# Kernel tuning notes

Measured on AMD Instinct MI355X. Metric: run time of the kernel, lower is better.

## Reference

```python
import jax, jax.numpy as jnp
import numpy as np

N = 1024
EMB = 128
FC = 512


def setup_inputs() -> dict:
    key = jax.random.key(0)
    ks = jax.random.split(key, 13)
    s = 0.05
    return {
        "x": jax.random.normal(ks[0], (N, 2), jnp.float32),
        "w_rel0": jax.random.normal(ks[1], (EMB, 2), jnp.float32) * s,
        "b_rel0": jax.random.normal(ks[2], (EMB,), jnp.float32) * s,
        "w_root0": jax.random.normal(ks[3], (EMB, 2), jnp.float32) * s,
        "w_rel1": jax.random.normal(ks[4], (EMB, EMB), jnp.float32) * s,
        "b_rel1": jax.random.normal(ks[5], (EMB,), jnp.float32) * s,
        "w_root1": jax.random.normal(ks[6], (EMB, EMB), jnp.float32) * s,
        "lw0": jax.random.normal(ks[7], (FC, EMB), jnp.float32) * s,
        "lb0": jax.random.normal(ks[8], (FC,), jnp.float32) * s,
        "lw1": jax.random.normal(ks[9], (FC, FC), jnp.float32) * s,
        "lb1": jax.random.normal(ks[10], (FC,), jnp.float32) * s,
        "lw2": jax.random.normal(ks[11], (1, FC), jnp.float32) * s,
        "lb2": jax.random.normal(ks[12], (1,), jnp.float32) * s,
    }


def _sage(x, w_rel, b_rel, w_root):
    # DenseSAGEConv with adj = all-ones NxN: neighbor mean == global mean.
    # out = lin_rel(adj@x / deg) + lin_root(x); lin_root has no bias.
    agg = jnp.mean(x, axis=0, keepdims=True)            # (1, d_in)
    return agg @ w_rel.T + b_rel + x @ w_root.T          # (N, d_out)


def reference(x, w_rel0, b_rel0, w_root0, w_rel1, b_rel1, w_root1,
              lw0, lb0, lw1, lb1, lw2, lb2):
    h = jax.nn.relu(_sage(x, w_rel0, b_rel0, w_root0))    # (N, EMB)
    h = jax.nn.relu(_sage(h, w_rel1, b_rel1, w_root1))    # (N, EMB)
    # triu(ones, 1).nonzero() -> all pairs i < j (static, N known at trace time)
    ei, ej = np.triu_indices(h.shape[0], 1)
    e = h[ei] * h[ej]                                     # (E, EMB)
    o = jax.nn.relu(e @ lw0.T + lb0)                      # (E, FC)
    o = jax.nn.relu(o @ lw1.T + lb1)                      # (E, FC)
    o = o @ lw2.T + lb2                                   # (E, 1)
    return jax.nn.sigmoid(o)[:, 0]                        # (E,)
```

## Files before the change

### kernel.cpp

```cpp
#include <hip/hip_runtime.h>
#include <hip/hip_bf16.h>
#include <math.h>

#define NN 1024
#define EMB 128
#define FC 512
#define NEDGE 523776
#define BM 64

typedef __attribute__((ext_vector_type(16))) float f32x16;
typedef __attribute__((ext_vector_type(8))) short bf16x8;
typedef __attribute__((ext_vector_type(4))) unsigned int u32x4;
typedef __attribute__((ext_vector_type(8))) int i32x8;

__device__ __forceinline__ float bf2f(unsigned short u) {
  union { unsigned int i; float f; } v; v.i = ((unsigned int)u) << 16; return v.f;
}
__device__ __forceinline__ unsigned short f2bf(float f) {
  return __builtin_bit_cast(unsigned short, __float2bfloat16(f));
}
__device__ __forceinline__ int cum_edges(int i) { return i * NN - ((i * (i + 1)) >> 1); }

__device__ __forceinline__ unsigned int pk4_fp8(float a, float b, float c, float d) {
  int v = __builtin_amdgcn_cvt_pk_fp8_f32(a, b, 0, false);
  v = __builtin_amdgcn_cvt_pk_fp8_f32(c, d, v, true);
  return (unsigned int)v;
}
#define MFMA32_L0(A,B,C) __builtin_amdgcn_mfma_scale_f32_32x32x64_f8f6f4((A),(B),(C),0,0,0,0x76767676,0,0x7f7f7f7f)
#define MFMA32_L1(A,B,C) __builtin_amdgcn_mfma_scale_f32_32x32x64_f8f6f4((A),(B),(C),0,0,0,0x72727272,0,0x7f7f7f7f)

__global__ void k_cvt_weights(const float* __restrict__ lw0, const float* __restrict__ lw1,
                              unsigned int* __restrict__ w0q, unsigned int* __restrict__ w1q) {
  int d = blockIdx.x * 256 + threadIdx.x;
  if (d < 16384) {
    int dw = d & 7, lane = (d >> 3) & 63, f = (d >> 9) & 1, kb = (d >> 10) & 1, wv = (d >> 11) & 7;
    int fc = wv*64 + f*32 + (lane & 31);
    int k  = kb*64 + (lane >> 5)*32 + dw*4;
    float4 s = *(const float4*)(lw0 + fc*EMB + k);
    w0q[d] = pk4_fp8(s.x*64.f, s.y*64.f, s.z*64.f, s.w*64.f);
  } else {
    int u = d - 16384;
    int dw = u & 7, lane = (u >> 3) & 63, f = (u >> 9) & 1, kb = (u >> 10) & 7, wv = (u >> 13) & 7;
    int fc = wv*64 + f*32 + (lane & 31);
    int k  = kb*64 + (lane >> 5)*32 + dw*4;
    float4 s = *(const float4*)(lw1 + fc*FC + k);
    w1q[u] = pk4_fp8(s.x*64.f, s.y*64.f, s.z*64.f, s.w*64.f);
  }
}

__global__ void k_mean_x(const float* __restrict__ x, float* __restrict__ mean0) {
  __shared__ float sx[256], sy[256];
  float ax = 0.f, ay = 0.f;
  for (int i = threadIdx.x; i < NN; i += 256) { ax += x[2*i]; ay += x[2*i+1]; }
  sx[threadIdx.x] = ax; sy[threadIdx.x] = ay;
  __syncthreads();
  for (int st = 128; st > 0; st >>= 1) {
    if (threadIdx.x < st) { sx[threadIdx.x] += sx[threadIdx.x+st]; sy[threadIdx.x] += sy[threadIdx.x+st]; }
    __syncthreads();
  }
  if (threadIdx.x == 0) { mean0[0] = sx[0] * (1.f/NN); mean0[1] = sy[0] * (1.f/NN); }
}

__global__ void k_sage0(const float* __restrict__ x, const float* __restrict__ wrel,
                        const float* __restrict__ brel, const float* __restrict__ wroot,
                        const float* __restrict__ mean0, float* __restrict__ h0) {
  int idx = blockIdx.x * 256 + threadIdx.x;
  int i = idx >> 7, c = idx & 127;
  float v = mean0[0]*wrel[2*c] + mean0[1]*wrel[2*c+1] + brel[c]
          + x[2*i]*wroot[2*c] + x[2*i+1]*wroot[2*c+1];
  h0[idx] = fmaxf(v, 0.f);
}

__global__ void k_mean_h0(const float* __restrict__ h0, float* __restrict__ mean1) {
  __shared__ float s[256];
  int c = blockIdx.x;
  float a = 0.f;
  for (int i = threadIdx.x; i < NN; i += 256) a += h0[i*EMB + c];
  s[threadIdx.x] = a;
  __syncthreads();
  for (int st = 128; st > 0; st >>= 1) {
    if (threadIdx.x < st) s[threadIdx.x] += s[threadIdx.x+st];
    __syncthreads();
  }
  if (threadIdx.x == 0) mean1[c] = s[0] * (1.f/NN);
}

__global__ void k_relc(const float* __restrict__ mean1, const float* __restrict__ wrel1,
                       const float* __restrict__ brel1, float* __restrict__ relc) {
  int c = threadIdx.x;
  float a = brel1[c];
  #pragma unroll 8
  for (int k = 0; k < EMB; ++k) a += mean1[k] * wrel1[c*EMB + k];
  relc[c] = a;
}

__global__ void k_sage1(const float* __restrict__ h0, const float* __restrict__ wroot1,
                        const float* __restrict__ relc, unsigned short* __restrict__ hb) {
  int idx = blockIdx.x * 256 + threadIdx.x;
  int i = idx >> 7, c = idx & 127;
  const float4* hr = (const float4*)(h0 + i*EMB);
  const float4* wr = (const float4*)(wroot1 + c*EMB);
  float a = relc[c];
  #pragma unroll 8
  for (int k = 0; k < EMB/4; ++k) {
    float4 h = hr[k], w = wr[k];
    a += h.x*w.x + h.y*w.y + h.z*w.z + h.w*w.w;
  }
  hb[idx] = f2bf(fmaxf(a, 0.f) * 32.0f);
}

__global__ __launch_bounds__(512, 4)
void k_edge_mlp(const unsigned short* __restrict__ hb,
                const unsigned int* __restrict__ w0q,
                const float* __restrict__ lb0,
                const unsigned int* __restrict__ w1q,
                const float* __restrict__ lb1,
                const float* __restrict__ lw2,
                const float* __restrict__ lb2,
                float* __restrict__ out) {
  __shared__ __align__(32) unsigned int e_lds[2048];
  __shared__ __align__(32) unsigned int o0_lds[8192];

  const int tid  = threadIdx.x;
  const int lane = tid & 63;
  const int wv   = tid >> 6;
  const int l31  = lane & 31;
  const int hi   = lane >> 5;
  const int blk  = blockIdx.x;
  const int fcb  = wv * 64;

  const char* w0w = (const char*)w0q + wv * 8192;
  const char* w1w = (const char*)w1q + wv * 32768;

  {
    int r = tid >> 3, q = tid & 7;
    int k = blk * BM + r;
    float s = sqrtf((float)(4190209 - 8*k));
    int i = (int)((2047.0f - s) * 0.5f);
    if (i < 0) i = 0;
    if (i > NN-2) i = NN-2;
    if (cum_edges(i+1) <= k) ++i;
    if (cum_edges(i+1) <= k) ++i;
    if (cum_edges(i) > k) --i;
    if (cum_edges(i) > k) --i;
    int j = k - cum_edges(i) + i + 1;
    const bf16x8* hi8 = (const bf16x8*)(hb + i*EMB + q*16);
    const bf16x8* hj8 = (const bf16x8*)(hb + j*EMB + q*16);
    float p[16];
    #pragma unroll
    for (int g = 0; g < 2; ++g) {
      bf16x8 a = hi8[g], b = hj8[g];
      #pragma unroll
      for (int u = 0; u < 8; ++u)
        p[g*8+u] = bf2f((unsigned short)a[u]) * bf2f((unsigned short)b[u]);
    }
    u32x4 d;
    #pragma unroll
    for (int u = 0; u < 4; ++u)
      d[u] = pk4_fp8(p[4*u], p[4*u+1], p[4*u+2], p[4*u+3]);
    int byt = (r>>5)*4096 + (q>>2)*2048 + ((q>>1)&1)*1024 + (r&31)*32 + (q&1)*16;
    *(u32x4*)((char*)e_lds + byt) = d;
  }
  __syncthreads();

  f32x16 acc[2][2];

  #pragma unroll
  for (int f = 0; f < 2; ++f)
    #pragma unroll
    for (int t = 0; t < 4; ++t) {
      float4 bv = *(const float4*)(lb0 + fcb + f*32 + t*8 + hi*4);
      #pragma unroll
      for (int e = 0; e < 2; ++e) {
        acc[e][f][4*t+0] = bv.x*128.f; acc[e][f][4*t+1] = bv.y*128.f;
        acc[e][f][4*t+2] = bv.z*128.f; acc[e][f][4*t+3] = bv.w*128.f;
      }
    }
  {
    const char* rbe = (const char*)e_lds + lane*32;
    #pragma unroll
    for (int kb = 0; kb < 2; ++kb) {
      i32x8 a0 = *(const i32x8*)(w0w + (kb*2+0)*2048 + lane*32);
      i32x8 a1 = *(const i32x8*)(w0w + (kb*2+1)*2048 + lane*32);
      i32x8 b0 = *(const i32x8*)(rbe + kb*2048);
      i32x8 b1 = *(const i32x8*)(rbe + 4096 + kb*2048);
      __builtin_amdgcn_s_setprio(1);
      acc[0][0] = MFMA32_L0(a0, b0, acc[0][0]);
      acc[0][1] = MFMA32_L0(a1, b0, acc[0][1]);
      acc[1][0] = MFMA32_L0(a0, b1, acc[1][0]);
      acc[1][1] = MFMA32_L0(a1, b1, acc[1][1]);
      __builtin_amdgcn_s_setprio(0);
    }
  }

  {
    char* ob = (char*)o0_lds + wv*2048 + l31*32 + hi*4;
    #pragma unroll
    for (int f = 0; f < 2; ++f)
      #pragma unroll
      for (int e = 0; e < 2; ++e)
        #pragma unroll
        for (int t = 0; t < 4; ++t) {
          unsigned int d = pk4_fp8(fmaxf(acc[e][f][4*t+0], 0.f),
                                   fmaxf(acc[e][f][4*t+1], 0.f),
                                   fmaxf(acc[e][f][4*t+2], 0.f),
                                   fmaxf(acc[e][f][4*t+3], 0.f));
          *(unsigned int*)(ob + e*16384 + f*1024 + t*8) = d;
        }
  }
  __syncthreads();

  #pragma unroll
  for (int f = 0; f < 2; ++f)
    #pragma unroll
    for (int t = 0; t < 4; ++t) {
      float4 bv = *(const float4*)(lb1 + fcb + f*32 + t*8 + hi*4);
      #pragma unroll
      for (int e = 0; e < 2; ++e) {
        acc[e][f][4*t+0] = bv.x; acc[e][f][4*t+1] = bv.y;
        acc[e][f][4*t+2] = bv.z; acc[e][f][4*t+3] = bv.w;
      }
    }
  {
    const char* rbo = (const char*)o0_lds + lane*32;
    #pragma unroll
    for (int kb = 0; kb < 8; ++kb) {
      i32x8 a0 = *(const i32x8*)(w1w + (kb*2+0)*2048 + lane*32);
      i32x8 a1 = *(const i32x8*)(w1w + (kb*2+1)*2048 + lane*32);
      i32x8 b0 = *(const i32x8*)(rbo + kb*2048);
      i32x8 b1 = *(const i32x8*)(rbo + 16384 + kb*2048);
      __builtin_amdgcn_s_setprio(1);
      acc[0][0] = MFMA32_L1(a0, b0, acc[0][0]);
      acc[0][1] = MFMA32_L1(a1, b0, acc[0][1]);
      acc[1][0] = MFMA32_L1(a0, b1, acc[1][0]);
      acc[1][1] = MFMA32_L1(a1, b1, acc[1][1]);
      __builtin_amdgcn_s_setprio(0);
    }
  }

  {
    float rs0 = 0.f, rs1 = 0.f;
    #pragma unroll
    for (int f = 0; f < 2; ++f)
      #pragma unroll
      for (int t = 0; t < 4; ++t) {
        float4 l2v = *(const float4*)(lw2 + fcb + f*32 + t*8 + hi*4);
        rs0 += fmaxf(acc[0][f][4*t+0], 0.f) * l2v.x;
        rs0 += fmaxf(acc[0][f][4*t+1], 0.f) * l2v.y;
        rs0 += fmaxf(acc[0][f][4*t+2], 0.f) * l2v.z;
        rs0 += fmaxf(acc[0][f][4*t+3], 0.f) * l2v.w;
        rs1 += fmaxf(acc[1][f][4*t+0], 0.f) * l2v.x;
        rs1 += fmaxf(acc[1][f][4*t+1], 0.f) * l2v.y;
        rs1 += fmaxf(acc[1][f][4*t+2], 0.f) * l2v.z;
        rs1 += fmaxf(acc[1][f][4*t+3], 0.f) * l2v.w;
      }
    rs0 += __shfl_xor(rs0, 32, 64);
    rs1 += __shfl_xor(rs1, 32, 64);
    float* red = (float*)e_lds;
    if (hi == 0) {
      red[wv*64 + l31]      = rs0;
      red[wv*64 + 32 + l31] = rs1;
    }
  }
  __syncthreads();

  if (tid < BM) {
    const float* red = (const float*)e_lds;
    float v = lb2[0];
    #pragma unroll
    for (int w = 0; w < 8; ++w) v += red[w*BM + tid];
    out[blk*BM + tid] = 1.0f / (1.0f + __expf(-v));
  }
}

extern "C" void kernel_launch(void* const* d_in, const int* in_sizes, int n_in,
                              void* d_out, int out_size, void* d_ws, size_t ws_size,
                              hipStream_t stream) {
  const float* x      = (const float*)d_in[0];
  const float* wrel0  = (const float*)d_in[1];
  const float* brel0  = (const float*)d_in[2];
  const float* wroot0 = (const float*)d_in[3];
  const float* wrel1  = (const float*)d_in[4];
  const float* brel1  = (const float*)d_in[5];
  const float* wroot1 = (const float*)d_in[6];
  const float* lw0    = (const float*)d_in[7];
  const float* lb0    = (const float*)d_in[8];
  const float* lw1    = (const float*)d_in[9];
  const float* lb1    = (const float*)d_in[10];
  const float* lw2    = (const float*)d_in[11];
  const float* lb2    = (const float*)d_in[12];
  float* out = (float*)d_out;

  char* ws = (char*)d_ws;
  unsigned short* hb  = (unsigned short*)(ws);
  unsigned int*   w0q = (unsigned int*)(ws + 262144);
  unsigned int*   w1q = (unsigned int*)(ws + 327680);
  float* h0    = (float*)(ws + 589824);
  float* mean0 = (float*)(ws + 1114112);
  float* mean1 = (float*)(ws + 1114176);
  float* relc  = (float*)(ws + 1114688);

  hipLaunchKernelGGL(k_cvt_weights, dim3(320), dim3(256), 0, stream, lw0, lw1, w0q, w1q);
  hipLaunchKernelGGL(k_mean_x,   dim3(1),    dim3(256), 0, stream, x, mean0);
  hipLaunchKernelGGL(k_sage0,    dim3(512),  dim3(256), 0, stream, x, wrel0, brel0, wroot0, mean0, h0);
  hipLaunchKernelGGL(k_mean_h0,  dim3(128),  dim3(256), 0, stream, h0, mean1);
  hipLaunchKernelGGL(k_relc,     dim3(1),    dim3(128), 0, stream, mean1, wrel1, brel1, relc);
  hipLaunchKernelGGL(k_sage1,    dim3(512),  dim3(256), 0, stream, h0, wroot1, relc, hb);
  hipLaunchKernelGGL(k_edge_mlp, dim3(NEDGE/BM), dim3(512), 0, stream,
                     hb, w0q, lb0, w1q, lb1, lw2, lb2, out);
}
```

Baseline: 198.9 us.

## Give each wave its own 64 edges, keeping MLP activations in registers

The edge MLP is restructured so that each wave owns 64 edges and computes every FC output column itself. Edge products and the layer-0 activations stay in registers, already in the fragment layout the next MFMA needs, so LDS staging and block barriers are gone. The weight pre-quantisation kernel is reordered so the fp8 layer-0 outputs feed layer 1 directly, and launch bounds drop to 2 blocks per SM. In exchange each wave now streams the full weight matrices from cache instead of a slice, and register pressure rises, which may lower occupancy.

New measurement: 226.1 us. 13.7% more time.

```diff
diff --git a/kernel.cpp b/kernel.cpp
--- a/kernel.cpp
+++ b/kernel.cpp
@@ -6,11 +6,9 @@
 #define EMB 128
 #define FC 512
 #define NEDGE 523776
-#define BM 64
 
 typedef __attribute__((ext_vector_type(16))) float f32x16;
 typedef __attribute__((ext_vector_type(8))) short bf16x8;
-typedef __attribute__((ext_vector_type(4))) unsigned int u32x4;
 typedef __attribute__((ext_vector_type(8))) int i32x8;
 
 __device__ __forceinline__ float bf2f(unsigned short u) {
@@ -33,18 +31,28 @@
                               unsigned int* __restrict__ w0q, unsigned int* __restrict__ w1q) {
   int d = blockIdx.x * 256 + threadIdx.x;
   if (d < 16384) {
-    int dw = d & 7, lane = (d >> 3) & 63, f = (d >> 9) & 1, kb = (d >> 10) & 1, wv = (d >> 11) & 7;
-    int fc = wv*64 + f*32 + (lane & 31);
-    int k  = kb*64 + (lane >> 5)*32 + dw*4;
-    float4 s = *(const float4*)(lw0 + fc*EMB + k);
-    w0q[d] = pk4_fp8(s.x*64.f, s.y*64.f, s.z*64.f, s.w*64.f);
+    int b4 = d & 7, lane = (d >> 3) & 63, kb0 = (d >> 9) & 1, mt = (d >> 10) & 15;
+    int fc = mt*32 + (lane & 31);
+    int kb = kb0*64 + (lane >> 5)*32 + b4*4;
+    float v0 = lw0[fc*EMB + kb + 0] * 64.f;
+    float v1 = lw0[fc*EMB + kb + 1] * 64.f;
+    float v2 = lw0[fc*EMB + kb + 2] * 64.f;
+    float v3 = lw0[fc*EMB + kb + 3] * 64.f;
+    w0q[d] = pk4_fp8(v0, v1, v2, v3);
   } else {
-    int u = d - 16384;
-    int dw = u & 7, lane = (u >> 3) & 63, f = (u >> 9) & 1, kb = (u >> 10) & 7, wv = (u >> 13) & 7;
-    int fc = wv*64 + f*32 + (lane & 31);
-    int k  = kb*64 + (lane >> 5)*32 + dw*4;
-    float4 s = *(const float4*)(lw1 + fc*FC + k);
-    w1q[u] = pk4_fp8(s.x*64.f, s.y*64.f, s.z*64.f, s.w*64.f);
+    int u_ = d - 16384;
+    int b4 = u_ & 7, lane = (u_ >> 3) & 63, kb1 = (u_ >> 9) & 7, mt1 = (u_ >> 12) & 15;
+    int h = lane >> 5;
+    int fc1 = mt1*32 + (lane & 31);
+    float v[4];
+    #pragma unroll
+    for (int u = 0; u < 4; ++u) {
+      int b = b4*4 + u;
+      int bb = b & 15;
+      int fc0 = kb1*64 + ((b >= 16) ? 32 : 0) + 4*h + (bb & 3) + 8*(bb >> 2);
+      v[u] = lw1[fc1*FC + fc0] * 64.f;
+    }
+    w1q[u_] = pk4_fp8(v[0], v[1], v[2], v[3]);
   }
 }
 
@@ -109,7 +117,7 @@
   hb[idx] = f2bf(fmaxf(a, 0.f) * 32.0f);
 }
 
-__global__ __launch_bounds__(512, 4)
+__global__ __launch_bounds__(512, 2)
 void k_edge_mlp(const unsigned short* __restrict__ hb,
                 const unsigned int* __restrict__ w0q,
                 const float* __restrict__ lb0,
@@ -118,23 +126,17 @@
                 const float* __restrict__ lw2,
                 const float* __restrict__ lb2,
                 float* __restrict__ out) {
-  __shared__ __align__(32) unsigned int e_lds[2048];
-  __shared__ __align__(32) unsigned int o0_lds[8192];
-
   const int tid  = threadIdx.x;
   const int lane = tid & 63;
   const int wv   = tid >> 6;
   const int l31  = lane & 31;
-  const int hi   = lane >> 5;
-  const int blk  = blockIdx.x;
-  const int fcb  = wv * 64;
-
-  const char* w0w = (const char*)w0q + wv * 8192;
-  const char* w1w = (const char*)w1q + wv * 32768;
-
-  {
-    int r = tid >> 3, q = tid & 7;
-    int k = blk * BM + r;
+  const int h    = lane >> 5;
+  const int ebase = blockIdx.x * 512 + wv * 64 + l31;
+
+  i32x8 ef[2][2];
+  #pragma unroll
+  for (int n = 0; n < 2; ++n) {
+    int k = ebase + n*32;
     float s = sqrtf((float)(4190209 - 8*k));
     int i = (int)((2047.0f - s) * 0.5f);
     if (i < 0) i = 0;
@@ -144,132 +146,90 @@
     if (cum_edges(i) > k) --i;
     if (cum_edges(i) > k) --i;
     int j = k - cum_edges(i) + i + 1;
-    const bf16x8* hi8 = (const bf16x8*)(hb + i*EMB + q*16);
-    const bf16x8* hj8 = (const bf16x8*)(hb + j*EMB + q*16);
-    float p[16];
-    #pragma unroll
-    for (int g = 0; g < 2; ++g) {
-      bf16x8 a = hi8[g], b = hj8[g];
+    #pragma unroll
+    for (int kb0 = 0; kb0 < 2; ++kb0) {
+      const bf16x8* pi = (const bf16x8*)(hb + i*EMB + kb0*64 + h*32);
+      const bf16x8* pj = (const bf16x8*)(hb + j*EMB + kb0*64 + h*32);
       #pragma unroll
-      for (int u = 0; u < 8; ++u)
-        p[g*8+u] = bf2f((unsigned short)a[u]) * bf2f((unsigned short)b[u]);
-    }
-    u32x4 d;
-    #pragma unroll
-    for (int u = 0; u < 4; ++u)
-      d[u] = pk4_fp8(p[4*u], p[4*u+1], p[4*u+2], p[4*u+3]);
-    int byt = (r>>5)*4096 + (q>>2)*2048 + ((q>>1)&1)*1024 + (r&31)*32 + (q&1)*16;
-    *(u32x4*)((char*)e_lds + byt) = d;
-  }
-  __syncthreads();
-
-  f32x16 acc[2][2];
-
+      for (int c = 0; c < 4; ++c) {
+        bf16x8 a = pi[c], b = pj[c];
+        float p[8];
+        #pragma unroll
+        for (int u = 0; u < 8; ++u)
+          p[u] = bf2f((unsigned short)a[u]) * bf2f((unsigned short)b[u]);
+        ef[n][kb0][c*2+0] = (int)pk4_fp8(p[0], p[1], p[2], p[3]);
+        ef[n][kb0][c*2+1] = (int)pk4_fp8(p[4], p[5], p[6], p[7]);
+      }
+    }
+  }
+
+  i32x8 o0f[2][8];
+  const char* w0c = (const char*)w0q;
   #pragma unroll
-  for (int f = 0; f < 2; ++f)
+  for (int mt = 0; mt < 16; ++mt) {
+    i32x8 wa = *(const i32x8*)(w0c + mt*4096 + lane*32);
+    i32x8 wb = *(const i32x8*)(w0c + mt*4096 + 2048 + lane*32);
+    f32x16 a0, a1;
     #pragma unroll
     for (int t = 0; t < 4; ++t) {
-      float4 bv = *(const float4*)(lb0 + fcb + f*32 + t*8 + hi*4);
-      #pragma unroll
-      for (int e = 0; e < 2; ++e) {
-        acc[e][f][4*t+0] = bv.x*128.f; acc[e][f][4*t+1] = bv.y*128.f;
-        acc[e][f][4*t+2] = bv.z*128.f; acc[e][f][4*t+3] = bv.w*128.f;
-      }
-    }
-  {
-    const char* rbe = (const char*)e_lds + lane*32;
-    #pragma unroll
-    for (int kb = 0; kb < 2; ++kb) {
-      i32x8 a0 = *(const i32x8*)(w0w + (kb*2+0)*2048 + lane*32);
-      i32x8 a1 = *(const i32x8*)(w0w + (kb*2+1)*2048 + lane*32);
-      i32x8 b0 = *(const i32x8*)(rbe + kb*2048);
-      i32x8 b1 = *(const i32x8*)(rbe + 4096 + kb*2048);
-      __builtin_amdgcn_s_setprio(1);
-      acc[0][0] = MFMA32_L0(a0, b0, acc[0][0]);
-      acc[0][1] = MFMA32_L0(a1, b0, acc[0][1]);
-      acc[1][0] = MFMA32_L0(a0, b1, acc[1][0]);
-      acc[1][1] = MFMA32_L0(a1, b1, acc[1][1]);
-      __builtin_amdgcn_s_setprio(0);
-    }
-  }
-
-  {
-    char* ob = (char*)o0_lds + wv*2048 + l31*32 + hi*4;
-    #pragma unroll
-    for (int f = 0; f < 2; ++f)
-      #pragma unroll
-      for (int e = 0; e < 2; ++e)
-        #pragma unroll
-        for (int t = 0; t < 4; ++t) {
-          unsigned int d = pk4_fp8(fmaxf(acc[e][f][4*t+0], 0.f),
-                                   fmaxf(acc[e][f][4*t+1], 0.f),
-                                   fmaxf(acc[e][f][4*t+2], 0.f),
-                                   fmaxf(acc[e][f][4*t+3], 0.f));
-          *(unsigned int*)(ob + e*16384 + f*1024 + t*8) = d;
-        }
-  }
-  __syncthreads();
-
+      float4 bv = *(const float4*)(lb0 + mt*32 + t*8 + h*4);
+      a0[4*t+0] = bv.x*128.f; a0[4*t+1] = bv.y*128.f;
+      a0[4*t+2] = bv.z*128.f; a0[4*t+3] = bv.w*128.f;
+      a1[4*t+0] = bv.x*128.f; a1[4*t+1] = bv.y*128.f;
+      a1[4*t+2] = bv.z*128.f; a1[4*t+3] = bv.w*128.f;
+    }
+    a0 = MFMA32_L0(wa, ef[0][0], a0);
+    a0 = MFMA32_L0(wb, ef[0][1], a0);
+    a1 = MFMA32_L0(wa, ef[1][0], a1);
+    a1 = MFMA32_L0(wb, ef[1][1], a1);
+    #pragma unroll
+    for (int d = 0; d < 4; ++d) {
+      o0f[0][mt>>1][(mt&1)*4 + d] = (int)pk4_fp8(
+          fmaxf(a0[4*d+0], 0.f), fmaxf(a0[4*d+1], 0.f),
+          fmaxf(a0[4*d+2], 0.f), fmaxf(a0[4*d+3], 0.f));
+      o0f[1][mt>>1][(mt&1)*4 + d] = (int)pk4_fp8(
+          fmaxf(a1[4*d+0], 0.f), fmaxf(a1[4*d+1], 0.f),
+          fmaxf(a1[4*d+2], 0.f), fmaxf(a1[4*d+3], 0.f));
+    }
+  }
+
+  float rs0 = 0.f, rs1 = 0.f;
+  const char* w1c = (const char*)w1q;
   #pragma unroll
-  for (int f = 0; f < 2; ++f)
+  for (int mt1 = 0; mt1 < 16; ++mt1) {
+    f32x16 a0, a1;
     #pragma unroll
     for (int t = 0; t < 4; ++t) {
-      float4 bv = *(const float4*)(lb1 + fcb + f*32 + t*8 + hi*4);
-      #pragma unroll
-      for (int e = 0; e < 2; ++e) {
-        acc[e][f][4*t+0] = bv.x; acc[e][f][4*t+1] = bv.y;
-        acc[e][f][4*t+2] = bv.z; acc[e][f][4*t+3] = bv.w;
-      }
-    }
-  {
-    const char* rbo = (const char*)o0_lds + lane*32;
-    #pragma unroll
-    for (int kb = 0; kb < 8; ++kb) {
-      i32x8 a0 = *(const i32x8*)(w1w + (kb*2+0)*2048 + lane*32);
-      i32x8 a1 = *(const i32x8*)(w1w + (kb*2+1)*2048 + lane*32);
-      i32x8 b0 = *(const i32x8*)(rbo + kb*2048);
-      i32x8 b1 = *(const i32x8*)(rbo + 16384 + kb*2048);
-      __builtin_amdgcn_s_setprio(1);
-      acc[0][0] = MFMA32_L1(a0, b0, acc[0][0]);
-      acc[0][1] = MFMA32_L1(a1, b0, acc[0][1]);
-      acc[1][0] = MFMA32_L1(a0, b1, acc[1][0]);
-      acc[1][1] = MFMA32_L1(a1, b1, acc[1][1]);
-      __builtin_amdgcn_s_setprio(0);
-    }
-  }
-
-  {
-    float rs0 = 0.f, rs1 = 0.f;
-    #pragma unroll
-    for (int f = 0; f < 2; ++f)
-      #pragma unroll
-      for (int t = 0; t < 4; ++t) {
-        float4 l2v = *(const float4*)(lw2 + fcb + f*32 + t*8 + hi*4);
-        rs0 += fmaxf(acc[0][f][4*t+0], 0.f) * l2v.x;
-        rs0 += fmaxf(acc[0][f][4*t+1], 0.f) * l2v.y;
-        rs0 += fmaxf(acc[0][f][4*t+2], 0.f) * l2v.z;
-        rs0 += fmaxf(acc[0][f][4*t+3], 0.f) * l2v.w;
-        rs1 += fmaxf(acc[1][f][4*t+0], 0.f) * l2v.x;
-        rs1 += fmaxf(acc[1][f][4*t+1], 0.f) * l2v.y;
-        rs1 += fmaxf(acc[1][f][4*t+2], 0.f) * l2v.z;
-        rs1 += fmaxf(acc[1][f][4*t+3], 0.f) * l2v.w;
-      }
-    rs0 += __shfl_xor(rs0, 32, 64);
-    rs1 += __shfl_xor(rs1, 32, 64);
-    float* red = (float*)e_lds;
-    if (hi == 0) {
-      red[wv*64 + l31]      = rs0;
-      red[wv*64 + 32 + l31] = rs1;
-    }
-  }
-  __syncthreads();
-
-  if (tid < BM) {
-    const float* red = (const float*)e_lds;
-    float v = lb2[0];
-    #pragma unroll
-    for (int w = 0; w < 8; ++w) v += red[w*BM + tid];
-    out[blk*BM + tid] = 1.0f / (1.0f + __expf(-v));
+      float4 bv = *(const float4*)(lb1 + mt1*32 + t*8 + h*4);
+      a0[4*t+0] = bv.x; a0[4*t+1] = bv.y; a0[4*t+2] = bv.z; a0[4*t+3] = bv.w;
+      a1[4*t+0] = bv.x; a1[4*t+1] = bv.y; a1[4*t+2] = bv.z; a1[4*t+3] = bv.w;
+    }
+    #pragma unroll
+    for (int kb1 = 0; kb1 < 8; ++kb1) {
+      i32x8 w = *(const i32x8*)(w1c + mt1*16384 + kb1*2048 + lane*32);
+      a0 = MFMA32_L1(w, o0f[0][kb1], a0);
+      a1 = MFMA32_L1(w, o0f[1][kb1], a1);
+    }
+    #pragma unroll
+    for (int t = 0; t < 4; ++t) {
+      float4 l2v = *(const float4*)(lw2 + mt1*32 + t*8 + h*4);
+      rs0 += fmaxf(a0[4*t+0], 0.f) * l2v.x;
+      rs0 += fmaxf(a0[4*t+1], 0.f) * l2v.y;
+      rs0 += fmaxf(a0[4*t+2], 0.f) * l2v.z;
+      rs0 += fmaxf(a0[4*t+3], 0.f) * l2v.w;
+      rs1 += fmaxf(a1[4*t+0], 0.f) * l2v.x;
+      rs1 += fmaxf(a1[4*t+1], 0.f) * l2v.y;
+      rs1 += fmaxf(a1[4*t+2], 0.f) * l2v.z;
+      rs1 += fmaxf(a1[4*t+3], 0.f) * l2v.w;
+    }
+  }
+
+  rs0 += __shfl_xor(rs0, 32, 64);
+  rs1 += __shfl_xor(rs1, 32, 64);
+  if (h == 0) {
+    float b2 = lb2[0];
+    out[ebase]      = 1.0f / (1.0f + __expf(-(rs0 + b2)));
+    out[ebase + 32] = 1.0f / (1.0f + __expf(-(rs1 + b2)));
   }
 }
 
@@ -306,6 +266,6 @@
   hipLaunchKernelGGL(k_mean_h0,  dim3(128),  dim3(256), 0, stream, h0, mean1);
   hipLaunchKernelGGL(k_relc,     dim3(1),    dim3(128), 0, stream, mean1, wrel1, brel1, relc);
   hipLaunchKernelGGL(k_sage1,    dim3(512),  dim3(256), 0, stream, h0, wroot1, relc, hb);
-  hipLaunchKernelGGL(k_edge_mlp, dim3(NEDGE/BM), dim3(512), 0, stream,
+  hipLaunchKernelGGL(k_edge_mlp, dim3(NEDGE/512), dim3(512), 0, stream,
                      hb, w0q, lb0, w1q, lb1, lw2, lb2, out);
 }
```
